# Performance work log

Hardware: AMD Instinct MI355X
Metric: run time of the kernel (lower is better)

Reference implementation:

```python
import jax, jax.numpy as jnp
import numpy as np

N = 50000       # nodes
E = 1600000     # edges (avg degree 32)
DIM = 256       # args.dim (input feature dim)
OUT = 64        # args.n_classes (output dim)
ALPHA = 0.2     # leaky relu negative slope


def setup_inputs() -> dict:
    key = jax.random.key(0)
    k1, k2, k3, k4 = jax.random.split(key, 4)
    x = jax.random.normal(k1, (N, DIM), dtype=jnp.float32)
    # sparse adjacency as COO indices: row 0 = src (output row), row 1 = dst (neighbor)
    edge_index = jax.random.randint(k2, (2, E), 0, N, dtype=jnp.int32)
    # xavier-uniform init as in SpGraphAttentionLayer
    lim_w = float(np.sqrt(6.0 / (DIM + OUT)))
    W = jax.random.uniform(k3, (DIM, OUT), minval=-lim_w, maxval=lim_w, dtype=jnp.float32)
    lim_a = float(np.sqrt(6.0 / (1 + 2 * OUT)))
    a = jax.random.uniform(k4, (2 * OUT,), minval=-lim_a, maxval=lim_a, dtype=jnp.float32)
    return {"x": x, "edge_index": edge_index, "W": W, "a": a}


def reference(x, edge_index, W, a):
    # h = x @ W : [N, OUT]
    h = x @ W
    src = edge_index[0]  # [E] output row index i
    dst = edge_index[1]  # [E] neighbor index j
    # attention logit per edge: a . concat(h[i], h[j])
    logits = h[src] @ a[:OUT] + h[dst] @ a[OUT:]          # [E]
    # edge_e = exp(-leakyrelu(logits))  (note the negation, as in SpGraphAttentionLayer)
    e = jnp.exp(-jax.nn.leaky_relu(logits, ALPHA))         # [E]
    # row-wise normalizer: sum_j e_ij
    rowsum = jax.ops.segment_sum(e, src, num_segments=N)   # [N]
    # aggregated messages: sum_j e_ij * h_j
    agg = jax.ops.segment_sum(e[:, None] * h[dst], src, num_segments=N)  # [N, OUT]
    # h' = agg / rowsum, then elu (concat=True branch)
    return jax.nn.elu(agg / rowsum[:, None])
```

## Files before the change

kernel.cpp:

```cpp
#include <hip/hip_runtime.h>

#define NN 50000
#define NE 1600000
#define DIM 256
#define OUTD 64
#define ALPHA 0.2f

#define BSH 6
#define NB ((NN + 63) >> 6)
#define CAP 3072
#define P1 1000
#define EPB (NE / P1)

#define GEMM_BLOCKS ((NN + 63) / 64)
#define WSTRIDE 264

typedef unsigned short u16;
typedef unsigned int u32;
typedef __attribute__((ext_vector_type(8))) short short8;
typedef __attribute__((ext_vector_type(4))) float floatx4;

__device__ __forceinline__ u16 f2bf(float f) {
  u32 b = __float_as_uint(f);
  b += 0x7FFFu + ((b >> 16) & 1u);
  return (u16)(b >> 16);
}
__device__ __forceinline__ float bflo(u32 u) { return __uint_as_float(u << 16); }
__device__ __forceinline__ float bfhi(u32 u) { return __uint_as_float(u & 0xFFFF0000u); }

__global__ __launch_bounds__(256) void init_kernel(const float* __restrict__ W,
                                                   u32* __restrict__ wt,
                                                   int* __restrict__ bktcnt) {
  if (blockIdx.x < 4) {
    const int i = blockIdx.x * 256 + threadIdx.x;
    if (i < NB) bktcnt[i] = 0;
    return;
  }
  const int g = (blockIdx.x - 4) * 256 + threadIdx.x;
  const int n = g >> 7;
  const int kp = g & 127;
  const float lo = W[(size_t)(2 * kp) * OUTD + n];
  const float hi = W[(size_t)(2 * kp + 1) * OUTD + n];
  wt[g] = (u32)f2bf(lo) | ((u32)f2bf(hi) << 16);
}

__global__ __launch_bounds__(256) void fat_kernel(
    const float* __restrict__ x, const u32* __restrict__ wt,
    const float* __restrict__ a, u16* __restrict__ hb,
    float* __restrict__ s1, float* __restrict__ s2,
    const int* __restrict__ src, const int* __restrict__ dst,
    int* __restrict__ bktcnt, u32* __restrict__ binned)
{
  __shared__ u16 Wl[OUTD * WSTRIDE];
  __shared__ int lh[NB];
  const int t = threadIdx.x;

  if (blockIdx.x < GEMM_BLOCKS) {
    {
      const uint4* srcv = (const uint4*)wt;
#pragma unroll
      for (int i = 0; i < 8; ++i) {
        const int c = t + 256 * i;
        const int n = c >> 5;
        const int k8 = c & 31;
        *(uint4*)&Wl[n * WSTRIDE + k8 * 8] = srcv[c];
      }
    }
    __syncthreads();

    const int lane = t & 63;
    const int wv = t >> 6;
    const int n = lane & 15;
    const int quad = lane >> 4;
    int rb = blockIdx.x * 64 + wv * 16;
    if (rb > NN - 16) rb = NN - 16;
    const int row = rb + n;
    const float4* xrow = (const float4*)(x + (size_t)row * DIM);

    floatx4 acc[4] = {{0.f, 0.f, 0.f, 0.f},
                      {0.f, 0.f, 0.f, 0.f},
                      {0.f, 0.f, 0.f, 0.f},
                      {0.f, 0.f, 0.f, 0.f}};

#pragma unroll
    for (int kk = 0; kk < 8; ++kk) {
      const float4 lo = xrow[kk * 8 + quad * 2];
      const float4 hi = xrow[kk * 8 + quad * 2 + 1];
      union { u32 u[4]; short8 s; } af;
      af.u[0] = (u32)f2bf(lo.x) | ((u32)f2bf(lo.y) << 16);
      af.u[1] = (u32)f2bf(lo.z) | ((u32)f2bf(lo.w) << 16);
      af.u[2] = (u32)f2bf(hi.x) | ((u32)f2bf(hi.y) << 16);
      af.u[3] = (u32)f2bf(hi.z) | ((u32)f2bf(hi.w) << 16);
#pragma unroll
      for (int nt = 0; nt < 4; ++nt) {
        const short8 bf =
            *(const short8*)&Wl[(nt * 16 + n) * WSTRIDE + kk * 32 + quad * 8];
        acc[nt] = __builtin_amdgcn_mfma_f32_16x16x32_bf16(af.s, bf, acc[nt], 0, 0, 0);
      }
    }

    float av1[4], av2[4];
#pragma unroll
    for (int nt = 0; nt < 4; ++nt) {
      av1[nt] = a[nt * 16 + n];
      av2[nt] = a[OUTD + nt * 16 + n];
    }

#pragma unroll
    for (int reg = 0; reg < 4; ++reg) {
      const int r = rb + quad * 4 + reg;
      float q1 = acc[0][reg] * av1[0] + acc[1][reg] * av1[1] +
                 acc[2][reg] * av1[2] + acc[3][reg] * av1[3];
      float q2 = acc[0][reg] * av2[0] + acc[1][reg] * av2[1] +
                 acc[2][reg] * av2[2] + acc[3][reg] * av2[3];
#pragma unroll
      for (int off = 1; off <= 8; off <<= 1) {
        q1 += __shfl_xor(q1, off);
        q2 += __shfl_xor(q2, off);
      }
      if (n == 0) { s1[r] = q1; s2[r] = q2; }
#pragma unroll
      for (int nt = 0; nt < 4; ++nt)
        hb[(size_t)r * OUTD + nt * 16 + n] = f2bf(acc[nt][reg]);
    }
    return;
  }

  const int p = blockIdx.x - GEMM_BLOCKS;
  for (int i = t; i < NB; i += 256) lh[i] = 0;
  __syncthreads();

  const int4* src4 = (const int4*)(src + p * EPB);
  const int4* dst4 = (const int4*)(dst + p * EPB);
  for (int i = t; i < EPB / 4; i += 256) {
    const int4 s = src4[i];
    if ((u32)s.x < (u32)NN) atomicAdd(&lh[s.x >> BSH], 1);
    if ((u32)s.y < (u32)NN) atomicAdd(&lh[s.y >> BSH], 1);
    if ((u32)s.z < (u32)NN) atomicAdd(&lh[s.z >> BSH], 1);
    if ((u32)s.w < (u32)NN) atomicAdd(&lh[s.w >> BSH], 1);
  }
  __syncthreads();

  for (int b = t; b < NB; b += 256) {
    const int c = lh[b];
    lh[b] = (c > 0) ? atomicAdd(bktcnt + b, c) + b * CAP : 0;
  }
  __syncthreads();

  for (int i = t; i < EPB / 4; i += 256) {
    const int4 s = src4[i];
    const int4 d = dst4[i];
    int pos, b;
    if ((u32)s.x < (u32)NN) {
      b = s.x >> BSH; pos = atomicAdd(&lh[b], 1);
      if (pos < (b + 1) * CAP) binned[pos] = ((u32)(s.x & 63) << 16) | (u32)(d.x & 0xFFFF);
    }
    if ((u32)s.y < (u32)NN) {
      b = s.y >> BSH; pos = atomicAdd(&lh[b], 1);
      if (pos < (b + 1) * CAP) binned[pos] = ((u32)(s.y & 63) << 16) | (u32)(d.y & 0xFFFF);
    }
    if ((u32)s.z < (u32)NN) {
      b = s.z >> BSH; pos = atomicAdd(&lh[b], 1);
      if (pos < (b + 1) * CAP) binned[pos] = ((u32)(s.z & 63) << 16) | (u32)(d.z & 0xFFFF);
    }
    if ((u32)s.w < (u32)NN) {
      b = s.w >> BSH; pos = atomicAdd(&lh[b], 1);
      if (pos < (b + 1) * CAP) binned[pos] = ((u32)(s.w & 63) << 16) | (u32)(d.w & 0xFFFF);
    }
  }
}

__global__ __launch_bounds__(256) void group_kernel(
    const u32* __restrict__ binned, const int* __restrict__ bktcnt,
    int* __restrict__ rowstart, int* __restrict__ deg,
    u16* __restrict__ edst16)
{
  __shared__ int cnt[64];
  __shared__ int off[64];
  const int b = blockIdx.x;
  const int t = threadIdx.x;
  int n = bktcnt[b];
  if (n > CAP) n = CAP;
  if (t < 64) cnt[t] = 0;
  __syncthreads();

  const u32* eb = binned + (size_t)b * CAP;
  for (int i = t; i < n; i += 256)
    atomicAdd(&cnt[(eb[i] >> 16) & 63], 1);
  __syncthreads();

  if (t < 64) {
    const int v = cnt[t];
    int xx = v;
#pragma unroll
    for (int o = 1; o < 64; o <<= 1) {
      const int y = __shfl_up(xx, o, 64);
      if (t >= o) xx += y;
    }
    off[t] = xx - v;
    const int node = b * 64 + t;
    if (node < NN) {
      rowstart[node] = b * CAP + xx - v;
      deg[node] = v;
    }
  }
  __syncthreads();

  for (int i = t; i < n; i += 256) {
    const u32 pv = eb[i];
    const int pos = atomicAdd(&off[(pv >> 16) & 63], 1);
    edst16[(size_t)b * CAP + pos] = (u16)(pv & 0xFFFFu);
  }
}

__global__ __launch_bounds__(256) void agg_kernel(
    const u16* __restrict__ hb, const float* __restrict__ s1,
    const float* __restrict__ s2, const int* __restrict__ pre,
    const int* __restrict__ deg, const u16* __restrict__ edst,
    float* __restrict__ out)
{
  const int lane = threadIdx.x & 63;
  const int g = lane >> 3;
  const int seg = lane & 7;
  const int node =
      __builtin_amdgcn_readfirstlane(blockIdx.x * 4 + (threadIdx.x >> 6));
  const int base = pre[node];
  const int cnt = deg[node];
  const float s1i = s1[node];

  float a0 = 0.f, a1 = 0.f, a2 = 0.f, a3 = 0.f;
  float a4 = 0.f, a5 = 0.f, a6 = 0.f, a7 = 0.f;
  float wsum = 0.f;

  for (int c0 = 0; c0 < cnt; c0 += 64) {
    const int m = min(64, cnt - c0);
    int d = 0;
    float w = 0.f;
    if (lane < m) {
      d = edst[(size_t)base + c0 + lane];
      const float logit = s1i + s2[d];
      const float lr = logit > 0.f ? logit : ALPHA * logit;
      w = __expf(-lr);
    }
#pragma unroll 4
    for (int e = 0; e < m; e += 8) {
      const int idx = e + g;
      const int dg = __shfl(d, idx);
      const float wg = __shfl(w, idx);
      const uint4 p = *(const uint4*)(hb + (size_t)dg * OUTD + seg * 8);
      a0 = fmaf(wg, bflo(p.x), a0);
      a1 = fmaf(wg, bfhi(p.x), a1);
      a2 = fmaf(wg, bflo(p.y), a2);
      a3 = fmaf(wg, bfhi(p.y), a3);
      a4 = fmaf(wg, bflo(p.z), a4);
      a5 = fmaf(wg, bfhi(p.z), a5);
      a6 = fmaf(wg, bflo(p.w), a6);
      a7 = fmaf(wg, bfhi(p.w), a7);
      wsum += wg;
    }
  }

#pragma unroll
  for (int off = 8; off <= 32; off <<= 1) {
    a0 += __shfl_xor(a0, off);
    a1 += __shfl_xor(a1, off);
    a2 += __shfl_xor(a2, off);
    a3 += __shfl_xor(a3, off);
    a4 += __shfl_xor(a4, off);
    a5 += __shfl_xor(a5, off);
    a6 += __shfl_xor(a6, off);
    a7 += __shfl_xor(a7, off);
    wsum += __shfl_xor(wsum, off);
  }

  if (g == 0) {
    const float inv = (cnt > 0) ? 1.f / wsum : 0.f;
    float4 r;
    float v;
    v = a0 * inv; r.x = v > 0.f ? v : (__expf(v) - 1.f);
    v = a1 * inv; r.y = v > 0.f ? v : (__expf(v) - 1.f);
    v = a2 * inv; r.z = v > 0.f ? v : (__expf(v) - 1.f);
    v = a3 * inv; r.w = v > 0.f ? v : (__expf(v) - 1.f);
    *(float4*)(out + (size_t)node * OUTD + seg * 8) = r;
    v = a4 * inv; r.x = v > 0.f ? v : (__expf(v) - 1.f);
    v = a5 * inv; r.y = v > 0.f ? v : (__expf(v) - 1.f);
    v = a6 * inv; r.z = v > 0.f ? v : (__expf(v) - 1.f);
    v = a7 * inv; r.w = v > 0.f ? v : (__expf(v) - 1.f);
    *(float4*)(out + (size_t)node * OUTD + seg * 8 + 4) = r;
  }
}

extern "C" void kernel_launch(void* const* d_in, const int* in_sizes, int n_in,
                              void* d_out, int out_size, void* d_ws, size_t ws_size,
                              hipStream_t stream) {
  const float* x = (const float*)d_in[0];
  const int* ei = (const int*)d_in[1];
  const float* W = (const float*)d_in[2];
  const float* a = (const float*)d_in[3];
  float* out = (float*)d_out;

  u16* hb = (u16*)d_ws;
  float* s1 = (float*)(hb + (size_t)NN * OUTD);
  float* s2 = s1 + NN;
  int* rowstart = (int*)(s2 + NN);
  int* deg = rowstart + NN;
  int* bktcnt = deg + NN;
  u32* wt = (u32*)(bktcnt + NB);
  u32* binned = wt + 8192;
  u16* edst16 = (u16*)(binned + (size_t)NB * CAP);

  const int* src = ei;
  const int* dst = ei + NE;

  hipLaunchKernelGGL(init_kernel, dim3(36), dim3(256), 0, stream, W, wt, bktcnt);
  hipLaunchKernelGGL(fat_kernel, dim3(GEMM_BLOCKS + P1), dim3(256), 0, stream,
                     x, wt, a, hb, s1, s2, src, dst, bktcnt, binned);
  hipLaunchKernelGGL(group_kernel, dim3(NB), dim3(256), 0, stream,
                     binned, bktcnt, rowstart, deg, edst16);
  hipLaunchKernelGGL(agg_kernel, dim3(NN / 4), dim3(256), 0, stream,
                     hb, s1, s2, rowstart, deg, edst16, out);
}
```

Measured before the change: 168.2 us.

## Interleave GEMM and binning blocks, drop init kernel, stage buckets in LDS

Removes the separate init kernel. Each GEMM block now converts W from fp32 to bf16 into LDS on its own, and bucket counts are cleared with a memset. The fat kernel's block IDs are interleaved so GEMM and edge-binning blocks are dispatched together, and the binning histogram reuses the W LDS buffer to cut LDS usage. The group kernel moves to 512 threads and caches its bucket in LDS so binned is read from global memory only once. Every GEMM block now repeats the W conversion with strided 2-byte LDS writes, which may cause bank conflicts.

```diff
diff --git a/kernel.cpp b/kernel.cpp
--- a/kernel.cpp
+++ b/kernel.cpp
@@ -14,6 +14,7 @@
 
 #define GEMM_BLOCKS ((NN + 63) / 64)
 #define WSTRIDE 264
+#define FAT_GRID 1782
 
 typedef unsigned short u16;
 typedef unsigned int u32;
@@ -28,51 +29,45 @@
 __device__ __forceinline__ float bflo(u32 u) { return __uint_as_float(u << 16); }
 __device__ __forceinline__ float bfhi(u32 u) { return __uint_as_float(u & 0xFFFF0000u); }
 
-__global__ __launch_bounds__(256) void init_kernel(const float* __restrict__ W,
-                                                   u32* __restrict__ wt,
-                                                   int* __restrict__ bktcnt) {
-  if (blockIdx.x < 4) {
-    const int i = blockIdx.x * 256 + threadIdx.x;
-    if (i < NB) bktcnt[i] = 0;
-    return;
-  }
-  const int g = (blockIdx.x - 4) * 256 + threadIdx.x;
-  const int n = g >> 7;
-  const int kp = g & 127;
-  const float lo = W[(size_t)(2 * kp) * OUTD + n];
-  const float hi = W[(size_t)(2 * kp + 1) * OUTD + n];
-  wt[g] = (u32)f2bf(lo) | ((u32)f2bf(hi) << 16);
-}
-
 __global__ __launch_bounds__(256) void fat_kernel(
-    const float* __restrict__ x, const u32* __restrict__ wt,
+    const float* __restrict__ x, const float* __restrict__ W,
     const float* __restrict__ a, u16* __restrict__ hb,
     float* __restrict__ s1, float* __restrict__ s2,
     const int* __restrict__ src, const int* __restrict__ dst,
     int* __restrict__ bktcnt, u32* __restrict__ binned)
 {
   __shared__ u16 Wl[OUTD * WSTRIDE];
-  __shared__ int lh[NB];
+  int* lh = (int*)Wl;
   const int t = threadIdx.x;
 
-  if (blockIdx.x < GEMM_BLOCKS) {
+  const int id = blockIdx.x;
+  int gb = -1, pb;
+  if (id & 1) pb = id >> 1;
+  else if ((id >> 1) < GEMM_BLOCKS) { gb = id >> 1; pb = -1; }
+  else pb = 891 + ((id - 2 * GEMM_BLOCKS) >> 1);
+
+  if (gb >= 0) {
     {
-      const uint4* srcv = (const uint4*)wt;
-#pragma unroll
-      for (int i = 0; i < 8; ++i) {
+      const float4* wv = (const float4*)W;
+#pragma unroll 4
+      for (int i = 0; i < 16; ++i) {
         const int c = t + 256 * i;
-        const int n = c >> 5;
-        const int k8 = c & 31;
-        *(uint4*)&Wl[n * WSTRIDE + k8 * 8] = srcv[c];
+        const int k = c >> 4;
+        const int n4 = (c & 15) * 4;
+        const float4 v = wv[c];
+        Wl[(n4 + 0) * WSTRIDE + k] = f2bf(v.x);
+        Wl[(n4 + 1) * WSTRIDE + k] = f2bf(v.y);
+        Wl[(n4 + 2) * WSTRIDE + k] = f2bf(v.z);
+        Wl[(n4 + 3) * WSTRIDE + k] = f2bf(v.w);
       }
     }
     __syncthreads();
 
     const int lane = t & 63;
-    const int wv = t >> 6;
+    const int wv_ = t >> 6;
     const int n = lane & 15;
     const int quad = lane >> 4;
-    int rb = blockIdx.x * 64 + wv * 16;
+    int rb = gb * 64 + wv_ * 16;
     if (rb > NN - 16) rb = NN - 16;
     const int row = rb + n;
     const float4* xrow = (const float4*)(x + (size_t)row * DIM);
@@ -126,7 +121,7 @@
     return;
   }
 
-  const int p = blockIdx.x - GEMM_BLOCKS;
+  const int p = pb;
   for (int i = t; i < NB; i += 256) lh[i] = 0;
   __syncthreads();
 
@@ -170,11 +165,12 @@
   }
 }
 
-__global__ __launch_bounds__(256) void group_kernel(
+__global__ __launch_bounds__(512) void group_kernel(
     const u32* __restrict__ binned, const int* __restrict__ bktcnt,
     int* __restrict__ rowstart, int* __restrict__ deg,
     u16* __restrict__ edst16)
 {
+  __shared__ u32 ebuf[CAP];
   __shared__ int cnt[64];
   __shared__ int off[64];
   const int b = blockIdx.x;
@@ -185,8 +181,11 @@
   __syncthreads();
 
   const u32* eb = binned + (size_t)b * CAP;
-  for (int i = t; i < n; i += 256)
-    atomicAdd(&cnt[(eb[i] >> 16) & 63], 1);
+  for (int i = t; i < n; i += 512) {
+    const u32 v = eb[i];
+    ebuf[i] = v;
+    atomicAdd(&cnt[(v >> 16) & 63], 1);
+  }
   __syncthreads();
 
   if (t < 64) {
@@ -206,8 +205,8 @@
   }
   __syncthreads();
 
-  for (int i = t; i < n; i += 256) {
-    const u32 pv = eb[i];
+  for (int i = t; i < n; i += 512) {
+    const u32 pv = ebuf[i];
     const int pos = atomicAdd(&off[(pv >> 16) & 63], 1);
     edst16[(size_t)b * CAP + pos] = (u16)(pv & 0xFFFFu);
   }
@@ -305,17 +304,16 @@
   int* rowstart = (int*)(s2 + NN);
   int* deg = rowstart + NN;
   int* bktcnt = deg + NN;
-  u32* wt = (u32*)(bktcnt + NB);
-  u32* binned = wt + 8192;
+  u32* binned = (u32*)(bktcnt + NB);
   u16* edst16 = (u16*)(binned + (size_t)NB * CAP);
 
   const int* src = ei;
   const int* dst = ei + NE;
 
-  hipLaunchKernelGGL(init_kernel, dim3(36), dim3(256), 0, stream, W, wt, bktcnt);
-  hipLaunchKernelGGL(fat_kernel, dim3(GEMM_BLOCKS + P1), dim3(256), 0, stream,
-                     x, wt, a, hb, s1, s2, src, dst, bktcnt, binned);
-  hipLaunchKernelGGL(group_kernel, dim3(NB), dim3(256), 0, stream,
+  hipMemsetAsync(bktcnt, 0, NB * sizeof(int), stream);
+  hipLaunchKernelGGL(fat_kernel, dim3(FAT_GRID), dim3(256), 0, stream,
+                     x, W, a, hb, s1, s2, src, dst, bktcnt, binned);
+  hipLaunchKernelGGL(group_kernel, dim3(NB), dim3(512), 0, stream,
                      binned, bktcnt, rowstart, deg, edst16);
   hipLaunchKernelGGL(agg_kernel, dim3(NN / 4), dim3(256), 0, stream,
                      hb, s1, s2, rowstart, deg, edst16, out);
```

After: 176.0 us. 1.05x slower.
